# Optimization experiments

Measured on AMD Instinct MI355X. Metric: run time of the kernel, lower is better.

## Reference

```python
import jax, jax.numpy as jnp
import numpy as np

T_MAX = 0.3  # clamp ceiling for effective opacity (t_max init kwarg)


def setup_inputs() -> dict:
    key = jax.random.key(0)
    k0, k1, k2 = jax.random.split(key, 3)
    B, n_blobs, d_s, d_f = 1024, 131072, 64, 256
    return {
        "query": jax.random.normal(k0, (B, d_s), dtype=jnp.float32),
        "mu": jax.random.normal(k1, (n_blobs, d_s), dtype=jnp.float32) * 0.02,
        "log_var": jnp.zeros((n_blobs, d_s), dtype=jnp.float32),
        "raw_alpha": jnp.zeros((n_blobs,), dtype=jnp.float32),
        "features": jax.random.normal(k2, (n_blobs, d_f), dtype=jnp.float32) * 0.02,
        "log_tau": jnp.asarray(np.log(128.0), dtype=jnp.float32),
        "k": 16,
    }


def reference(query, mu, log_var, raw_alpha, features, log_tau, k):
    # query: [B, d_s]; mu/log_var: [N, d_s]; features: [N, d_f]
    tau = jnp.exp(log_tau)
    inv_var = jnp.exp(-log_var)                              # [N, d_s]
    # Mahalanobis distance expanded to avoid the [B, N, d_s] diff tensor:
    # sum_d (q - mu)^2 * iv = q^2.iv - 2 q.(mu*iv) + sum(mu^2*iv)
    q2 = jnp.einsum('bd,nd->bn', query * query, inv_var)      # [B, N]
    cross = jnp.einsum('bd,nd->bn', query, mu * inv_var)      # [B, N]
    m2 = jnp.sum(mu * mu * inv_var, axis=-1)                  # [N]
    mahal = q2 - 2.0 * cross + m2[None, :]
    K_all = jnp.exp(-0.5 * mahal / tau)                       # [B, N]
    alpha = jax.nn.sigmoid(raw_alpha)                         # [N]
    scores = K_all * alpha[None, :]
    top_scores, top_idx = jax.lax.top_k(scores, k)            # [B, k]

    # Gather selected blobs and recompute exact kernel (as in the original render)
    blob_feats = features[top_idx]                            # [B, k, d_f]
    blob_mu = mu[top_idx]                                     # [B, k, d_s]
    blob_iv = jnp.exp(-log_var[top_idx])                      # [B, k, d_s]
    diff = query[:, None, :] - blob_mu                        # [B, k, d_s]
    mahal_k = jnp.sum(diff * diff * blob_iv, axis=-1)         # [B, k]
    K_topk = jnp.exp(-0.5 * mahal_k / tau)
    blob_alpha = alpha[top_idx]                               # [B, k]

    # Alpha compositing in log space
    eff = jnp.minimum(blob_alpha * K_topk, T_MAX / k)         # [B, k]
    log_1m = jnp.log1p(-jnp.minimum(eff, 1.0 - 1e-6))
    log_cum = jnp.cumsum(log_1m, axis=-1)
    log_T = jnp.concatenate(
        [jnp.zeros_like(log_cum[:, :1]), log_cum[:, :-1]], axis=-1)
    weights = eff * jnp.exp(log_T)                            # [B, k]
    blob_meaning = jnp.einsum('bk,bkd->bd', weights, blob_feats)  # [B, d_f]
    t_residual = jnp.exp(log_cum[:, -1])                      # [B]
    return blob_meaning, t_residual
```

## Files before the change

### kernel.cpp

```cpp
#include <hip/hip_runtime.h>
#include <math.h>

#define BQ    1024
#define NB    131072
#define DS    64
#define DF    256
#define KSEL  16

#define QT    128
#define BC    64
#define PCH   64
#define NCHUNK (NB / BC)
#define CHUNKS_PER_BLK (NCHUNK/PCH)
#define CPQ   (PCH * KSEL)
#define SLD   68

#define CH_BYTES   32768
#define SPLIT_OFF  16384

typedef __bf16 bf16x8 __attribute__((ext_vector_type(8)));
typedef float  f32x4  __attribute__((ext_vector_type(4)));
typedef unsigned long long u64;

#define ENC_NEGINF 0x007FFFFFu

__device__ __forceinline__ unsigned map_f32(float s) {
    unsigned u = __float_as_uint(s);
    return (u & 0x80000000u) ? ~u : (u | 0x80000000u);
}

__device__ __forceinline__ float unmap_f32(unsigned e) {
    return __uint_as_float((e & 0x80000000u) ? (e & 0x7FFFFFFFu) : ~e);
}

__device__ __forceinline__ void async_cp16(const void* g, void* l) {
    __builtin_amdgcn_global_load_lds(
        (const __attribute__((address_space(1))) unsigned int*)g,
        (__attribute__((address_space(3))) unsigned int*)l, 16, 0, 0);
}

__global__ __launch_bounds__(256)
void prep_kernel(const float* __restrict__ mu,
                 const float* __restrict__ log_var,
                 const float* __restrict__ raw_alpha,
                 char* __restrict__ bprep,
                 float* __restrict__ m2la,
                 unsigned* __restrict__ gcut)
{
    int gid  = blockIdx.x * 256 + threadIdx.x;
    if (gid < BQ) gcut[gid] = ENC_NEGINF;
    int blob = gid >> 3;
    int dd   = gid & 7;

    const float* mrow = mu      + (size_t)blob * DS + dd * 8;
    const float* vrow = log_var + (size_t)blob * DS + dd * 8;
    float4 ma = ((const float4*)mrow)[0], mb = ((const float4*)mrow)[1];
    float4 va = ((const float4*)vrow)[0], vb = ((const float4*)vrow)[1];
    float m[8] = {ma.x, ma.y, ma.z, ma.w, mb.x, mb.y, mb.z, mb.w};
    float lv[8] = {va.x, va.y, va.z, va.w, vb.x, vb.y, vb.z, vb.w};

    bf16x8 hiv, liv, hmv, lmv;
    float p = 0.0f;
    #pragma unroll
    for (int j = 0; j < 8; ++j) {
        float iv = __expf(-lv[j]);
        float mv = m[j] * iv;
        p += m[j] * mv;
        __bf16 h1 = (__bf16)iv;  hiv[j] = h1; liv[j] = (__bf16)(iv - (float)h1);
        __bf16 h2 = (__bf16)mv;  hmv[j] = h2; lmv[j] = (__bf16)(mv - (float)h2);
    }
    p += __shfl_xor(p, 1);
    p += __shfl_xor(p, 2);
    p += __shfl_xor(p, 4);

    int c  = blob >> 6;
    int nt = (blob >> 4) & 3;
    int bl = blob & 15;
    int lane  = (dd & 3) * 16 + bl;
    int ks_iv = dd >> 2;
    int ks_mv = 2 + (dd >> 2);
    size_t b_iv = (size_t)c * CH_BYTES + nt * 4096 + ks_iv * 1024 + lane * 16;
    size_t b_mv = (size_t)c * CH_BYTES + nt * 4096 + ks_mv * 1024 + lane * 16;
    *(bf16x8*)(bprep + b_iv)             = hiv;
    *(bf16x8*)(bprep + b_iv + SPLIT_OFF) = liv;
    *(bf16x8*)(bprep + b_mv)             = hmv;
    *(bf16x8*)(bprep + b_mv + SPLIT_OFF) = lmv;

    if (dd == 0) {
        m2la[blob * 2]     = p;
        m2la[blob * 2 + 1] = -log1pf(__expf(-raw_alpha[blob]));
    }
}

__device__ __forceinline__ void ins16(float (&ts)[16], int (&ti)[16],
                                      float& mymin, float s, int idx)
{
    float v0[8]; int j0[8];
    #pragma unroll
    for (int i = 0; i < 8; ++i) {
        bool b = ts[2*i+1] < ts[2*i];
        v0[i] = b ? ts[2*i+1] : ts[2*i];
        j0[i] = (i << 1) | (b ? 1 : 0);
    }
    float v1[4]; int j1[4];
    #pragma unroll
    for (int i = 0; i < 4; ++i) {
        bool b = v0[2*i+1] < v0[2*i];
        v1[i] = b ? v0[2*i+1] : v0[2*i];
        j1[i] = b ? j0[2*i+1] : j0[2*i];
    }
    float v2[2]; int j2[2];
    #pragma unroll
    for (int i = 0; i < 2; ++i) {
        bool b = v1[2*i+1] < v1[2*i];
        v2[i] = b ? v1[2*i+1] : v1[2*i];
        j2[i] = b ? j1[2*i+1] : j1[2*i];
    }
    int am = (v2[1] < v2[0]) ? j2[1] : j2[0];
    #pragma unroll
    for (int i = 0; i < 16; ++i) {
        bool b = (i == am);
        ts[i] = b ? s : ts[i];
        ti[i] = b ? idx : ti[i];
    }
    float n0[8];
    #pragma unroll
    for (int i = 0; i < 8; ++i) n0[i] = fminf(ts[2*i], ts[2*i+1]);
    float n1[4];
    #pragma unroll
    for (int i = 0; i < 4; ++i) n1[i] = fminf(n0[2*i], n0[2*i+1]);
    mymin = fminf(fminf(n1[0], n1[1]), fminf(n1[2], n1[3]));
}

__global__ __launch_bounds__(256, 2)
void score_topk_kernel(const float* __restrict__ query,
                       const char* __restrict__ bprep,
                       const float* __restrict__ m2la,
                       const float* __restrict__ log_tau_p,
                       u64* __restrict__ cand,
                       unsigned* __restrict__ gcut)
{
    __shared__ __align__(16) short Bs[CH_BYTES / 2];
    __shared__ __align__(16) float St[QT * SLD];
    __shared__ float scv[2 * QT];

    const int tid   = threadIdx.x;
    const int lane  = tid & 63;
    const int quad  = lane >> 4;
    const int mrow  = lane & 15;
    const int wv    = tid >> 6;
    const int qbase = blockIdx.y * QT;

    const float nhit = -0.5f * expf(-log_tau_p[0]);

    bf16x8 ahi[2][4], alo[2][4];
    #pragma unroll
    for (int mt = 0; mt < 2; ++mt) {
        const float* qrow = query + (size_t)(qbase + wv * 32 + mt * 16 + mrow) * DS;
        #pragma unroll
        for (int ks = 0; ks < 4; ++ks) {
            int kq = ks * 32 + quad * 8;
            int d0 = kq & 63;
            bool lin = kq >= 64;
            bf16x8 h, l;
            #pragma unroll
            for (int j = 0; j < 8; ++j) {
                float v = qrow[d0 + j];
                float x = lin ? (-2.0f * v) : (v * v);
                __bf16 hb = (__bf16)x;
                h[j] = hb;
                l[j] = (__bf16)(x - (float)hb);
            }
            ahi[mt][ks] = h; alo[mt][ks] = l;
        }
    }

    float ts[16]; int ti[16];
    #pragma unroll
    for (int i = 0; i < 16; ++i) { ts[i] = -INFINITY; ti[i] = 0; }
    float mymin = -INFINITY;
    const int qloc = tid & 127;
    const int half = tid >> 7;
    if (tid < 2 * QT) scv[tid] = -INFINITY;
    unsigned* const gslot = gcut + qbase + qloc;

    const char* BsB = (const char*)Bs;

    int c = blockIdx.x;
    {
        const char* src = bprep + (size_t)c * CH_BYTES;
        #pragma unroll
        for (int i = 0; i < 8; ++i) {
            int s = tid + i * 256;
            async_cp16(src + s * 16, (void*)(BsB + s * 16));
        }
    }
    __syncthreads();

    for (int it = 0; it < CHUNKS_PER_BLK; ++it) {
        const int nbase = c * BC;
        const int cn    = c + PCH;
        const bool more = (it + 1) < CHUNKS_PER_BLK;

        unsigned eg = atomicMax(gslot, map_f32(mymin));

        float2 ml[4];
        #pragma unroll
        for (int nt = 0; nt < 4; ++nt)
            ml[nt] = *(const float2*)&m2la[(size_t)(nbase + nt * 16 + mrow) * 2];

        f32x4 acc[2][4];
        #pragma unroll
        for (int nt = 0; nt < 4; ++nt) {
            bf16x8 bh[4], bl[4];
            #pragma unroll
            for (int ks = 0; ks < 4; ++ks) {
                bh[ks] = *(const bf16x8*)(BsB + nt * 4096 + ks * 1024 + lane * 16);
                bl[ks] = *(const bf16x8*)(BsB + SPLIT_OFF + nt * 4096 + ks * 1024 + lane * 16);
            }
            #pragma unroll
            for (int mt = 0; mt < 2; ++mt) {
                f32x4 a = {0.0f, 0.0f, 0.0f, 0.0f};
                #pragma unroll
                for (int ks = 0; ks < 4; ++ks) {
                    a = __builtin_amdgcn_mfma_f32_16x16x32_bf16(ahi[mt][ks], bh[ks], a, 0, 0, 0);
                    a = __builtin_amdgcn_mfma_f32_16x16x32_bf16(ahi[mt][ks], bl[ks], a, 0, 0, 0);
                    a = __builtin_amdgcn_mfma_f32_16x16x32_bf16(alo[mt][ks], bh[ks], a, 0, 0, 0);
                }
                acc[mt][nt] = a;
            }
        }
        __syncthreads();

        if (more) {
            const char* src = bprep + (size_t)cn * CH_BYTES;
            #pragma unroll
            for (int i = 0; i < 8; ++i) {
                int s = tid + i * 256;
                async_cp16(src + s * 16, (void*)(BsB + s * 16));
            }
        }

        #pragma unroll
        for (int mt = 0; mt < 2; ++mt)
            #pragma unroll
            for (int nt = 0; nt < 4; ++nt) {
                float m2 = ml[nt].x, la = ml[nt].y;
                #pragma unroll
                for (int reg = 0; reg < 4; ++reg) {
                    float sc = nhit * (acc[mt][nt][reg] + m2) + la;
                    St[(wv * 32 + mt * 16 + quad * 4 + reg) * SLD + nt * 16 + mrow] = sc;
                }
            }
        __syncthreads();

        {
            volatile float* vsc = scv;
            float ocut = vsc[(half ^ 1) * QT + qloc];
            float gc   = unmap_f32(eg);
            float bcut = fmaxf(ocut, gc);
            float cut  = fmaxf(mymin, bcut);
            const float* rowp = &St[qloc * SLD + half * 32];
            unsigned gm = 0u;
            #pragma unroll
            for (int i = 0; i < 8; ++i) {
                float4 v = ((const float4*)rowp)[i];
                float mx = fmaxf(fmaxf(v.x, v.y), fmaxf(v.z, v.w));
                if (mx > cut) gm |= (1u << i);
            }
            while (__any(gm != 0u)) {
                if (gm) {
                    int i = __ffs(gm) - 1;
                    gm &= gm - 1u;
                    float4 v = ((const float4*)rowp)[i];
                    int b0 = nbase + half * 32 + i * 4;
                    if (v.x > cut) { ins16(ts, ti, mymin, v.x, b0);     cut = fmaxf(mymin, bcut); }
                    if (v.y > cut) { ins16(ts, ti, mymin, v.y, b0 + 1); cut = fmaxf(mymin, bcut); }
                    if (v.z > cut) { ins16(ts, ti, mymin, v.z, b0 + 2); cut = fmaxf(mymin, bcut); }
                    if (v.w > cut) { ins16(ts, ti, mymin, v.w, b0 + 3); cut = fmaxf(mymin, bcut); }
                }
            }
            vsc[half * QT + qloc] = mymin;
        }
        __syncthreads();
        c = cn;
    }
    __syncthreads();

    u64* SK = (u64*)St;
    #pragma unroll
    for (int i = 0; i < 16; ++i)
        SK[qloc * 33 + half * 16 + i] =
            ((u64)map_f32(ts[i]) << 32) | (u64)(0xFFFFFFFFu - (unsigned)ti[i]);
    __syncthreads();

    if (tid < QT) {
        u64* row = SK + tid * 33;
        u64* dst = cand + (size_t)(qbase + tid) * CPQ + blockIdx.x * KSEL;
        for (int r = 0; r < KSEL; ++r) {
            int bm = 0; u64 bv = row[0];
            #pragma unroll 4
            for (int j = 1; j < 32; ++j) { u64 v = row[j]; if (v > bv) { bv = v; bm = j; } }
            row[bm] = 0;
            dst[r] = bv;
        }
    }
}

__global__ __launch_bounds__(256)
void merge_composite_kernel(const float* __restrict__ query,
                            const float* __restrict__ mu,
                            const float* __restrict__ log_var,
                            const float* __restrict__ raw_alpha,
                            const float* __restrict__ features,
                            const float* __restrict__ log_tau_p,
                            const u64* __restrict__ cand,
                            float* __restrict__ out)
{
    const int q   = blockIdx.x;
    const int tid = threadIdx.x;
    const int wv = tid >> 6, lane = tid & 63;

    __shared__ u64   wtop[4 * KSEL];
    __shared__ int   sel[KSEL];
    __shared__ float w_sh[KSEL];
    __shared__ float mah[KSEL];
    __shared__ float alp[KSEL];

    u64 k[4];
    #pragma unroll
    for (int r = 0; r < 4; ++r)
        k[r] = cand[(size_t)q * CPQ + wv * 256 + r * 64 + lane];

    for (int r = 0; r < KSEL; ++r) {
        u64 m = k[0];
        #pragma unroll
        for (int j = 1; j < 4; ++j) if (k[j] > m) m = k[j];
        #pragma unroll
        for (int off = 32; off > 0; off >>= 1) {
            unsigned hi = __shfl_xor((unsigned)(m >> 32), off);
            unsigned lo = __shfl_xor((unsigned)(m & 0xFFFFFFFFu), off);
            u64 o = ((u64)hi << 32) | lo;
            if (o > m) m = o;
        }
        if (lane == 0) wtop[wv * KSEL + r] = m;
        #pragma unroll
        for (int j = 0; j < 4; ++j) if (k[j] == m) k[j] = 0ull;
    }
    __syncthreads();

    if (wv == 0) {
        u64 kk = wtop[lane];
        for (int r = 0; r < KSEL; ++r) {
            u64 m = kk;
            #pragma unroll
            for (int off = 32; off > 0; off >>= 1) {
                unsigned hi = __shfl_xor((unsigned)(m >> 32), off);
                unsigned lo = __shfl_xor((unsigned)(m & 0xFFFFFFFFu), off);
                u64 o = ((u64)hi << 32) | lo;
                if (o > m) m = o;
            }
            if (kk == m) kk = 0ull;
            if (lane == 0)
                sel[r] = (int)(0xFFFFFFFFu - (unsigned)(m & 0xFFFFFFFFull));
        }
    }
    __syncthreads();

    for (int r = wv; r < KSEL; r += 4) {
        int bi = sel[r];
        float qd = query[(size_t)q * DS + lane];
        float mv = mu[(size_t)bi * DS + lane];
        float d  = qd - mv;
        float t  = d * d * expf(-log_var[(size_t)bi * DS + lane]);
        #pragma unroll
        for (int off = 32; off > 0; off >>= 1) t += __shfl_down(t, off);
        if (lane == 0) {
            mah[r] = t;
            alp[r] = 1.0f / (1.0f + expf(-raw_alpha[bi]));
        }
    }
    __syncthreads();

    if (tid == 0) {
        float tau = expf(log_tau_p[0]);
        float cap = 0.3f / 16.0f;
        float logT = 0.0f;
        for (int r = 0; r < KSEL; ++r) {
            float K   = expf(-0.5f * mah[r] / tau);
            float eff = fminf(alp[r] * K, cap);
            w_sh[r]   = eff * expf(logT);
            logT     += log1pf(-fminf(eff, 1.0f - 1e-6f));
        }
        out[(size_t)BQ * DF + q] = expf(logT);
    }
    __syncthreads();

    {
        float a = 0.0f;
        #pragma unroll
        for (int r = 0; r < KSEL; ++r)
            a += w_sh[r] * features[(size_t)sel[r] * DF + tid];
        out[(size_t)q * DF + tid] = a;
    }
}

extern "C" void kernel_launch(void* const* d_in, const int* in_sizes, int n_in,
                              void* d_out, int out_size, void* d_ws, size_t ws_size,
                              hipStream_t stream)
{
    (void)in_sizes; (void)n_in; (void)out_size; (void)ws_size;
    const float* query     = (const float*)d_in[0];
    const float* mu        = (const float*)d_in[1];
    const float* log_var   = (const float*)d_in[2];
    const float* raw_alpha = (const float*)d_in[3];
    const float* features  = (const float*)d_in[4];
    const float* log_tau   = (const float*)d_in[5];
    float* out = (float*)d_out;

    char*  bprep = (char*)d_ws;
    float* m2la  = (float*)((char*)d_ws + (size_t)NCHUNK * CH_BYTES);
    u64*   cand  = (u64*)((char*)d_ws + (size_t)NCHUNK * CH_BYTES + (size_t)NB * 2 * 4);
    unsigned* gcut = (unsigned*)(out + (size_t)BQ * DF);

    prep_kernel<<<(NB * 8) / 256, 256, 0, stream>>>(mu, log_var, raw_alpha, bprep, m2la, gcut);

    dim3 g2(PCH, BQ / QT);
    score_topk_kernel<<<g2, 256, 0, stream>>>(query, bprep, m2la, log_tau, cand, gcut);

    merge_composite_kernel<<<BQ, 256, 0, stream>>>(query, mu, log_var, raw_alpha,
                                                   features, log_tau, cand, out);
}
```

Measured before the change: 602.3 us.

## Filter top-k candidates via shared queue instead of full score staging

After the MFMA scoring, each lane compares its scores against a per-query cutoff held in shared memory. Only scores above the cutoff go into a shared-memory queue through atomics, and a single owner thread per query scans that queue. The full-tile store to shared memory plus the two-half scan is kept only for the cold first iteration and for queue overflow. The final 32-to-16 reduction per block is dropped because one owner thread now holds all 16 entries, and the candidate layout changes to per-block-major. The intent is to cut shared-memory traffic and top-k scan work once cutoffs are tight. In exchange, the owner threads scan the whole queue serially, and half the threads sit idle during insertion.

```diff
diff --git a/kernel.cpp b/kernel.cpp
--- a/kernel.cpp
+++ b/kernel.cpp
@@ -12,8 +12,8 @@
 #define PCH   64
 #define NCHUNK (NB / BC)
 #define CHUNKS_PER_BLK (NCHUNK/PCH)
-#define CPQ   (PCH * KSEL)
 #define SLD   68
+#define QCAP  512
 
 #define CH_BYTES   32768
 #define SPLIT_OFF  16384
@@ -142,7 +142,9 @@
 {
     __shared__ __align__(16) short Bs[CH_BYTES / 2];
     __shared__ __align__(16) float St[QT * SLD];
-    __shared__ float scv[2 * QT];
+    __shared__ __align__(16) float cutF[QT];
+    __shared__ __align__(16) u64  qent[QCAP];
+    __shared__ int qcnt[2];
 
     const int tid   = threadIdx.x;
     const int lane  = tid & 63;
@@ -179,10 +181,11 @@
     #pragma unroll
     for (int i = 0; i < 16; ++i) { ts[i] = -INFINITY; ti[i] = 0; }
     float mymin = -INFINITY;
-    const int qloc = tid & 127;
-    const int half = tid >> 7;
-    if (tid < 2 * QT) scv[tid] = -INFINITY;
-    unsigned* const gslot = gcut + qbase + qloc;
+    const bool owner = tid < QT;
+    unsigned* const gslot = gcut + qbase + (tid & (QT - 1));
+
+    if (tid < QT) cutF[tid] = -INFINITY;
+    if (tid == 0) { qcnt[0] = 0; qcnt[1] = 0; }
 
     const char* BsB = (const char*)Bs;
 
@@ -201,8 +204,10 @@
         const int nbase = c * BC;
         const int cn    = c + PCH;
         const bool more = (it + 1) < CHUNKS_PER_BLK;
-
-        unsigned eg = atomicMax(gslot, map_f32(mymin));
+        const int p     = it & 1;
+
+        unsigned eg = 0;
+        if (owner) eg = atomicMax(gslot, map_f32(mymin));
 
         float2 ml[4];
         #pragma unroll
@@ -240,70 +245,109 @@
                 async_cp16(src + s * 16, (void*)(BsB + s * 16));
             }
         }
-
-        #pragma unroll
-        for (int mt = 0; mt < 2; ++mt)
-            #pragma unroll
-            for (int nt = 0; nt < 4; ++nt) {
-                float m2 = ml[nt].x, la = ml[nt].y;
+        if (tid == 0) qcnt[p ^ 1] = 0;
+
+        f32x4 cf0 = *(const f32x4*)&cutF[wv * 32 + quad * 4];
+        f32x4 cf1 = *(const f32x4*)&cutF[wv * 32 + 16 + quad * 4];
+        bool cold = (cf0[0] == -INFINITY);
+
+        if (cold) {
+            if (tid == 0) qcnt[p] = 1 << 20;
+        } else {
+            float mx = -1.0f;
+            #pragma unroll
+            for (int mt = 0; mt < 2; ++mt)
                 #pragma unroll
-                for (int reg = 0; reg < 4; ++reg) {
-                    float sc = nhit * (acc[mt][nt][reg] + m2) + la;
-                    St[(wv * 32 + mt * 16 + quad * 4 + reg) * SLD + nt * 16 + mrow] = sc;
+                for (int nt = 0; nt < 4; ++nt) {
+                    float m2 = ml[nt].x, la = ml[nt].y;
+                    #pragma unroll
+                    for (int reg = 0; reg < 4; ++reg) {
+                        float sc  = nhit * (acc[mt][nt][reg] + m2) + la;
+                        float cfv = (mt == 0) ? cf0[reg] : cf1[reg];
+                        mx = fmaxf(mx, sc - cfv);
+                    }
                 }
-            }
+            if (__any(mx > 0.0f)) {
+                #pragma unroll
+                for (int mt = 0; mt < 2; ++mt)
+                    #pragma unroll
+                    for (int nt = 0; nt < 4; ++nt) {
+                        float m2 = ml[nt].x, la = ml[nt].y;
+                        #pragma unroll
+                        for (int reg = 0; reg < 4; ++reg) {
+                            float sc  = nhit * (acc[mt][nt][reg] + m2) + la;
+                            float cfv = (mt == 0) ? cf0[reg] : cf1[reg];
+                            if (sc > cfv) {
+                                int slot = atomicAdd(&qcnt[p], 1);
+                                if (slot < QCAP) {
+                                    int row = wv * 32 + mt * 16 + quad * 4 + reg;
+                                    int col = nt * 16 + mrow;
+                                    qent[slot] = ((u64)__float_as_uint(sc) << 32)
+                                               | (unsigned)((row << 6) | col);
+                                }
+                            }
+                        }
+                    }
+            }
+        }
         __syncthreads();
 
-        {
-            volatile float* vsc = scv;
-            float ocut = vsc[(half ^ 1) * QT + qloc];
-            float gc   = unmap_f32(eg);
-            float bcut = fmaxf(ocut, gc);
-            float cut  = fmaxf(mymin, bcut);
-            const float* rowp = &St[qloc * SLD + half * 32];
-            unsigned gm = 0u;
-            #pragma unroll
-            for (int i = 0; i < 8; ++i) {
-                float4 v = ((const float4*)rowp)[i];
-                float mx = fmaxf(fmaxf(v.x, v.y), fmaxf(v.z, v.w));
-                if (mx > cut) gm |= (1u << i);
-            }
-            while (__any(gm != 0u)) {
-                if (gm) {
-                    int i = __ffs(gm) - 1;
-                    gm &= gm - 1u;
+        const int L = qcnt[p];
+        const float gc = unmap_f32(eg);
+
+        if (L > QCAP) {
+            #pragma unroll
+            for (int mt = 0; mt < 2; ++mt)
+                #pragma unroll
+                for (int nt = 0; nt < 4; ++nt) {
+                    float m2 = ml[nt].x, la = ml[nt].y;
+                    #pragma unroll
+                    for (int reg = 0; reg < 4; ++reg) {
+                        float sc = nhit * (acc[mt][nt][reg] + m2) + la;
+                        St[(wv * 32 + mt * 16 + quad * 4 + reg) * SLD + nt * 16 + mrow] = sc;
+                    }
+                }
+            __syncthreads();
+            if (owner) {
+                float cut = fmaxf(mymin, gc);
+                const float* rowp = &St[tid * SLD];
+                #pragma unroll
+                for (int i = 0; i < 16; ++i) {
                     float4 v = ((const float4*)rowp)[i];
-                    int b0 = nbase + half * 32 + i * 4;
-                    if (v.x > cut) { ins16(ts, ti, mymin, v.x, b0);     cut = fmaxf(mymin, bcut); }
-                    if (v.y > cut) { ins16(ts, ti, mymin, v.y, b0 + 1); cut = fmaxf(mymin, bcut); }
-                    if (v.z > cut) { ins16(ts, ti, mymin, v.z, b0 + 2); cut = fmaxf(mymin, bcut); }
-                    if (v.w > cut) { ins16(ts, ti, mymin, v.w, b0 + 3); cut = fmaxf(mymin, bcut); }
+                    float m4 = fmaxf(fmaxf(v.x, v.y), fmaxf(v.z, v.w));
+                    if (m4 > cut) {
+                        int b0 = nbase + i * 4;
+                        if (v.x > cut) { ins16(ts, ti, mymin, v.x, b0);     cut = fmaxf(mymin, gc); }
+                        if (v.y > cut) { ins16(ts, ti, mymin, v.y, b0 + 1); cut = fmaxf(mymin, gc); }
+                        if (v.z > cut) { ins16(ts, ti, mymin, v.z, b0 + 2); cut = fmaxf(mymin, gc); }
+                        if (v.w > cut) { ins16(ts, ti, mymin, v.w, b0 + 3); cut = fmaxf(mymin, gc); }
+                    }
                 }
             }
-            vsc[half * QT + qloc] = mymin;
-        }
-        __syncthreads();
+        } else if (owner && L > 0) {
+            float cut = fmaxf(mymin, gc);
+            for (int j = 0; j < L; ++j) {
+                u64 e = qent[j];
+                int rc = (int)(e & 0xFFFFFFFFu);
+                if ((rc >> 6) == tid) {
+                    float s = __uint_as_float((unsigned)(e >> 32));
+                    if (s > cut) {
+                        ins16(ts, ti, mymin, s, nbase + (rc & 63));
+                        cut = fmaxf(mymin, gc);
+                    }
+                }
+            }
+        }
+
+        if (owner) cutF[tid] = fmaxf(mymin, gc);
         c = cn;
     }
-    __syncthreads();
-
-    u64* SK = (u64*)St;
-    #pragma unroll
-    for (int i = 0; i < 16; ++i)
-        SK[qloc * 33 + half * 16 + i] =
-            ((u64)map_f32(ts[i]) << 32) | (u64)(0xFFFFFFFFu - (unsigned)ti[i]);
-    __syncthreads();
-
-    if (tid < QT) {
-        u64* row = SK + tid * 33;
-        u64* dst = cand + (size_t)(qbase + tid) * CPQ + blockIdx.x * KSEL;
-        for (int r = 0; r < KSEL; ++r) {
-            int bm = 0; u64 bv = row[0];
-            #pragma unroll 4
-            for (int j = 1; j < 32; ++j) { u64 v = row[j]; if (v > bv) { bv = v; bm = j; } }
-            row[bm] = 0;
-            dst[r] = bv;
-        }
+
+    if (owner) {
+        u64* dst = cand + ((size_t)blockIdx.x * BQ + qbase + tid) * KSEL;
+        #pragma unroll
+        for (int r = 0; r < KSEL; ++r)
+            dst[r] = ((u64)map_f32(ts[r]) << 32) | (u64)(0xFFFFFFFFu - (unsigned)ti[r]);
     }
 }
 
@@ -329,8 +373,10 @@
 
     u64 k[4];
     #pragma unroll
-    for (int r = 0; r < 4; ++r)
-        k[r] = cand[(size_t)q * CPQ + wv * 256 + r * 64 + lane];
+    for (int r = 0; r < 4; ++r) {
+        int g = wv * 256 + r * 64 + lane;
+        k[r] = cand[((size_t)(g >> 4) * BQ + q) * KSEL + (g & 15)];
+    }
 
     for (int r = 0; r < KSEL; ++r) {
         u64 m = k[0];
```

New measurement: 1.639 ms. +172.1%, slower.

## Keep scores in registers and do per-lane top-k selection without LDS staging

Applied to the files above, without the earlier changes.

The MFMA operands are swapped so each lane holds scores for a single query row. That lets the score transform, threshold test and top-16 insertion run directly on accumulator registers, removing the shared-memory score tile and its extra block barriers. Each lane now keeps two private top-16 lists. These are reduced across quads with shuffles, and the candidate buffer layout changes to chunk-major, with the merge kernel's indexing updated to match. The cost is higher register pressure and a 16-way select (mux) when extracting a flagged score. Each lane also now scans 16 candidates per row where the old code used a split-half scheme.

```diff
diff --git a/kernel.cpp b/kernel.cpp
--- a/kernel.cpp
+++ b/kernel.cpp
@@ -12,8 +12,6 @@
 #define PCH   64
 #define NCHUNK (NB / BC)
 #define CHUNKS_PER_BLK (NCHUNK/PCH)
-#define CPQ   (PCH * KSEL)
-#define SLD   68
 
 #define CH_BYTES   32768
 #define SPLIT_OFF  16384
@@ -132,6 +130,24 @@
     mymin = fminf(fminf(n1[0], n1[1]), fminf(n1[2], n1[3]));
 }
 
+__device__ __forceinline__ float mux16(const f32x4 (&a)[4], int i)
+{
+    float v = a[0][0];
+    v = (i == 1)  ? a[0][1] : v;  v = (i == 2)  ? a[0][2] : v;  v = (i == 3)  ? a[0][3] : v;
+    v = (i == 4)  ? a[1][0] : v;  v = (i == 5)  ? a[1][1] : v;  v = (i == 6)  ? a[1][2] : v;
+    v = (i == 7)  ? a[1][3] : v;  v = (i == 8)  ? a[2][0] : v;  v = (i == 9)  ? a[2][1] : v;
+    v = (i == 10) ? a[2][2] : v;  v = (i == 11) ? a[2][3] : v;  v = (i == 12) ? a[3][0] : v;
+    v = (i == 13) ? a[3][1] : v;  v = (i == 14) ? a[3][2] : v;  v = (i == 15) ? a[3][3] : v;
+    return v;
+}
+
+__device__ __forceinline__ u64 shflxor64(u64 m, int mask)
+{
+    unsigned hi = __shfl_xor((unsigned)(m >> 32), mask);
+    unsigned lo = __shfl_xor((unsigned)(m & 0xFFFFFFFFu), mask);
+    return ((u64)hi << 32) | lo;
+}
+
 __global__ __launch_bounds__(256, 2)
 void score_topk_kernel(const float* __restrict__ query,
                        const char* __restrict__ bprep,
@@ -141,8 +157,6 @@
                        unsigned* __restrict__ gcut)
 {
     __shared__ __align__(16) short Bs[CH_BYTES / 2];
-    __shared__ __align__(16) float St[QT * SLD];
-    __shared__ float scv[2 * QT];
 
     const int tid   = threadIdx.x;
     const int lane  = tid & 63;
@@ -175,14 +189,15 @@
         }
     }
 
-    float ts[16]; int ti[16];
-    #pragma unroll
-    for (int i = 0; i < 16; ++i) { ts[i] = -INFINITY; ti[i] = 0; }
-    float mymin = -INFINITY;
-    const int qloc = tid & 127;
-    const int half = tid >> 7;
-    if (tid < 2 * QT) scv[tid] = -INFINITY;
-    unsigned* const gslot = gcut + qbase + qloc;
+    float ts0[16], ts1[16]; int ti0[16], ti1[16];
+    #pragma unroll
+    for (int i = 0; i < 16; ++i) {
+        ts0[i] = -INFINITY; ti0[i] = 0;
+        ts1[i] = -INFINITY; ti1[i] = 0;
+    }
+    float my0 = -INFINITY, my1 = -INFINITY;
+    unsigned* const gs0 = gcut + qbase + wv * 32 + mrow;
+    unsigned* const gs1 = gcut + qbase + wv * 32 + 16 + mrow;
 
     const char* BsB = (const char*)Bs;
 
@@ -202,12 +217,20 @@
         const int cn    = c + PCH;
         const bool more = (it + 1) < CHUNKS_PER_BLK;
 
-        unsigned eg = atomicMax(gslot, map_f32(mymin));
-
-        float2 ml[4];
-        #pragma unroll
-        for (int nt = 0; nt < 4; ++nt)
-            ml[nt] = *(const float2*)&m2la[(size_t)(nbase + nt * 16 + mrow) * 2];
+        float p0 = my0;
+        p0 = fmaxf(p0, __shfl_xor(p0, 16)); p0 = fmaxf(p0, __shfl_xor(p0, 32));
+        float p1 = my1;
+        p1 = fmaxf(p1, __shfl_xor(p1, 16)); p1 = fmaxf(p1, __shfl_xor(p1, 32));
+        unsigned e0 = ENC_NEGINF, e1 = ENC_NEGINF;
+        if (quad == 0) e0 = atomicMax(gs0, map_f32(p0));
+        if (quad == 1) e1 = atomicMax(gs1, map_f32(p1));
+
+        float4 mlA[4], mlB[4];
+        #pragma unroll
+        for (int nt = 0; nt < 4; ++nt) {
+            const float4* mp = (const float4*)&m2la[(size_t)(nbase + nt * 16 + quad * 4) * 2];
+            mlA[nt] = mp[0]; mlB[nt] = mp[1];
+        }
 
         f32x4 acc[2][4];
         #pragma unroll
@@ -223,9 +246,9 @@
                 f32x4 a = {0.0f, 0.0f, 0.0f, 0.0f};
                 #pragma unroll
                 for (int ks = 0; ks < 4; ++ks) {
-                    a = __builtin_amdgcn_mfma_f32_16x16x32_bf16(ahi[mt][ks], bh[ks], a, 0, 0, 0);
-                    a = __builtin_amdgcn_mfma_f32_16x16x32_bf16(ahi[mt][ks], bl[ks], a, 0, 0, 0);
-                    a = __builtin_amdgcn_mfma_f32_16x16x32_bf16(alo[mt][ks], bh[ks], a, 0, 0, 0);
+                    a = __builtin_amdgcn_mfma_f32_16x16x32_bf16(bh[ks], ahi[mt][ks], a, 0, 0, 0);
+                    a = __builtin_amdgcn_mfma_f32_16x16x32_bf16(bl[ks], ahi[mt][ks], a, 0, 0, 0);
+                    a = __builtin_amdgcn_mfma_f32_16x16x32_bf16(bh[ks], alo[mt][ks], a, 0, 0, 0);
                 }
                 acc[mt][nt] = a;
             }
@@ -241,69 +264,103 @@
             }
         }
 
-        #pragma unroll
-        for (int mt = 0; mt < 2; ++mt)
+        unsigned ee0 = __shfl(e0, mrow);
+        unsigned ee1 = __shfl(e1, 16 + mrow);
+        const float gc0 = fmaxf(unmap_f32(ee0), p0);
+        const float gc1 = fmaxf(unmap_f32(ee1), p1);
+
+        {
+            float cut = fmaxf(my0, gc0);
+            unsigned gm = 0u;
             #pragma unroll
             for (int nt = 0; nt < 4; ++nt) {
-                float m2 = ml[nt].x, la = ml[nt].y;
-                #pragma unroll
-                for (int reg = 0; reg < 4; ++reg) {
-                    float sc = nhit * (acc[mt][nt][reg] + m2) + la;
-                    St[(wv * 32 + mt * 16 + quad * 4 + reg) * SLD + nt * 16 + mrow] = sc;
-                }
-            }
-        __syncthreads();
-
-        {
-            volatile float* vsc = scv;
-            float ocut = vsc[(half ^ 1) * QT + qloc];
-            float gc   = unmap_f32(eg);
-            float bcut = fmaxf(ocut, gc);
-            float cut  = fmaxf(mymin, bcut);
-            const float* rowp = &St[qloc * SLD + half * 32];
-            unsigned gm = 0u;
-            #pragma unroll
-            for (int i = 0; i < 8; ++i) {
-                float4 v = ((const float4*)rowp)[i];
-                float mx = fmaxf(fmaxf(v.x, v.y), fmaxf(v.z, v.w));
-                if (mx > cut) gm |= (1u << i);
+                float m2_0 = mlA[nt].x, la_0 = mlA[nt].y;
+                float m2_1 = mlA[nt].z, la_1 = mlA[nt].w;
+                float m2_2 = mlB[nt].x, la_2 = mlB[nt].y;
+                float m2_3 = mlB[nt].z, la_3 = mlB[nt].w;
+                float s0 = nhit * (acc[0][nt][0] + m2_0) + la_0;
+                float s1 = nhit * (acc[0][nt][1] + m2_1) + la_1;
+                float s2 = nhit * (acc[0][nt][2] + m2_2) + la_2;
+                float s3 = nhit * (acc[0][nt][3] + m2_3) + la_3;
+                acc[0][nt][0] = s0; acc[0][nt][1] = s1;
+                acc[0][nt][2] = s2; acc[0][nt][3] = s3;
+                if (s0 > cut) gm |= 1u << (nt * 4);
+                if (s1 > cut) gm |= 1u << (nt * 4 + 1);
+                if (s2 > cut) gm |= 1u << (nt * 4 + 2);
+                if (s3 > cut) gm |= 1u << (nt * 4 + 3);
             }
             while (__any(gm != 0u)) {
                 if (gm) {
-                    int i = __ffs(gm) - 1;
-                    gm &= gm - 1u;
-                    float4 v = ((const float4*)rowp)[i];
-                    int b0 = nbase + half * 32 + i * 4;
-                    if (v.x > cut) { ins16(ts, ti, mymin, v.x, b0);     cut = fmaxf(mymin, bcut); }
-                    if (v.y > cut) { ins16(ts, ti, mymin, v.y, b0 + 1); cut = fmaxf(mymin, bcut); }
-                    if (v.z > cut) { ins16(ts, ti, mymin, v.z, b0 + 2); cut = fmaxf(mymin, bcut); }
-                    if (v.w > cut) { ins16(ts, ti, mymin, v.w, b0 + 3); cut = fmaxf(mymin, bcut); }
+                    int i = __ffs(gm) - 1; gm &= gm - 1u;
+                    float s = mux16(acc[0], i);
+                    if (s > cut) {
+                        ins16(ts0, ti0, my0, s, nbase + (i >> 2) * 16 + quad * 4 + (i & 3));
+                        cut = fmaxf(my0, gc0);
+                    }
                 }
             }
-            vsc[half * QT + qloc] = mymin;
-        }
+        }
+        {
+            float cut = fmaxf(my1, gc1);
+            unsigned gm = 0u;
+            #pragma unroll
+            for (int nt = 0; nt < 4; ++nt) {
+                float m2_0 = mlA[nt].x, la_0 = mlA[nt].y;
+                float m2_1 = mlA[nt].z, la_1 = mlA[nt].w;
+                float m2_2 = mlB[nt].x, la_2 = mlB[nt].y;
+                float m2_3 = mlB[nt].z, la_3 = mlB[nt].w;
+                float s0 = nhit * (acc[1][nt][0] + m2_0) + la_0;
+                float s1 = nhit * (acc[1][nt][1] + m2_1) + la_1;
+                float s2 = nhit * (acc[1][nt][2] + m2_2) + la_2;
+                float s3 = nhit * (acc[1][nt][3] + m2_3) + la_3;
+                acc[1][nt][0] = s0; acc[1][nt][1] = s1;
+                acc[1][nt][2] = s2; acc[1][nt][3] = s3;
+                if (s0 > cut) gm |= 1u << (nt * 4);
+                if (s1 > cut) gm |= 1u << (nt * 4 + 1);
+                if (s2 > cut) gm |= 1u << (nt * 4 + 2);
+                if (s3 > cut) gm |= 1u << (nt * 4 + 3);
+            }
+            while (__any(gm != 0u)) {
+                if (gm) {
+                    int i = __ffs(gm) - 1; gm &= gm - 1u;
+                    float s = mux16(acc[1], i);
+                    if (s > cut) {
+                        ins16(ts1, ti1, my1, s, nbase + (i >> 2) * 16 + quad * 4 + (i & 3));
+                        cut = fmaxf(my1, gc1);
+                    }
+                }
+            }
+        }
+
         __syncthreads();
         c = cn;
     }
-    __syncthreads();
-
-    u64* SK = (u64*)St;
-    #pragma unroll
-    for (int i = 0; i < 16; ++i)
-        SK[qloc * 33 + half * 16 + i] =
-            ((u64)map_f32(ts[i]) << 32) | (u64)(0xFFFFFFFFu - (unsigned)ti[i]);
-    __syncthreads();
-
-    if (tid < QT) {
-        u64* row = SK + tid * 33;
-        u64* dst = cand + (size_t)(qbase + tid) * CPQ + blockIdx.x * KSEL;
-        for (int r = 0; r < KSEL; ++r) {
-            int bm = 0; u64 bv = row[0];
-            #pragma unroll 4
-            for (int j = 1; j < 32; ++j) { u64 v = row[j]; if (v > bv) { bv = v; bm = j; } }
-            row[bm] = 0;
-            dst[r] = bv;
-        }
+
+    #pragma unroll
+    for (int mt = 0; mt < 2; ++mt) {
+        u64 k[16];
+        #pragma unroll
+        for (int i = 0; i < 16; ++i) {
+            float  tsv = (mt == 0) ? ts0[i] : ts1[i];
+            int    tiv = (mt == 0) ? ti0[i] : ti1[i];
+            k[i] = ((u64)map_f32(tsv) << 32) | (u64)(0xFFFFFFFFu - (unsigned)tiv);
+        }
+        u64 outv[4];
+        #pragma unroll
+        for (int r = 0; r < 16; ++r) {
+            u64 m = k[0];
+            #pragma unroll
+            for (int j = 1; j < 16; ++j) if (k[j] > m) m = k[j];
+            u64 o = shflxor64(m, 16); if (o > m) m = o;
+            o = shflxor64(m, 32);     if (o > m) m = o;
+            #pragma unroll
+            for (int j = 0; j < 16; ++j) if (k[j] == m) k[j] = 0ull;
+            if ((r & 3) == quad) outv[r >> 2] = m;
+        }
+        u64* dst = cand + ((size_t)blockIdx.x * BQ + qbase + wv * 32 + mt * 16 + mrow) * KSEL;
+        #pragma unroll
+        for (int j = 0; j < 4; ++j)
+            dst[quad + 4 * j] = outv[j];
     }
 }
 
@@ -329,8 +386,10 @@
 
     u64 k[4];
     #pragma unroll
-    for (int r = 0; r < 4; ++r)
-        k[r] = cand[(size_t)q * CPQ + wv * 256 + r * 64 + lane];
+    for (int r = 0; r < 4; ++r) {
+        int g = wv * 256 + r * 64 + lane;
+        k[r] = cand[((size_t)(g >> 4) * BQ + q) * KSEL + (g & 15)];
+    }
 
     for (int r = 0; r < KSEL; ++r) {
         u64 m = k[0];
```

Measured after the change: 622.2 us. 3.3% more time.
